# Kernel optimization log

Measured on AMD Instinct MI355X. Metric: run time of the kernel, lower is better.

Reference implementation:

```python
import jax, jax.numpy as jnp
import numpy as np

T, B, H, L = 256, 64, 1024, 2

def setup_inputs() -> dict:
    key = jax.random.key(0)
    ks = jax.random.split(key, 7)
    s = 1.0 / np.sqrt(H)  # torch LSTMCell init scale (uniform); randn*s keeps magnitudes sane
    return {
        "input_seq": jax.random.normal(ks[0], (T, B, H), jnp.float32),
        "h0": jax.random.normal(ks[1], (L, B, H), jnp.float32),
        "c0": jax.random.normal(ks[2], (L, B, H), jnp.float32),
        "W_ih": jax.random.normal(ks[3], (L, 4 * H, H), jnp.float32) * s,
        "W_hh": jax.random.normal(ks[4], (L, 4 * H, H), jnp.float32) * s,
        "b_ih": jax.random.normal(ks[5], (L, 4 * H), jnp.float32) * s,
        "b_hh": jax.random.normal(ks[6], (L, 4 * H), jnp.float32) * s,
    }

def _lstm_cell(x, h, c, w_ih, w_hh, bi, bh):
    # torch.nn.LSTMCell gate order: i, f, g, o
    gates = x @ w_ih.T + bi + h @ w_hh.T + bh  # [B, 4H]
    i, f, g, o = jnp.split(gates, 4, axis=-1)
    c_new = jax.nn.sigmoid(f) * c + jax.nn.sigmoid(i) * jnp.tanh(g)
    h_new = jax.nn.sigmoid(o) * jnp.tanh(c_new)
    return h_new, c_new

def reference(input_seq, h0, c0, W_ih, W_hh, b_ih, b_hh):
    def step(carry, x_t):
        h, c = carry  # each [L, B, H]
        new_h, new_c = [], []
        x = x_t
        for l in range(L):  # small fixed layer loop
            hl, cl = _lstm_cell(x, h[l], c[l], W_ih[l], W_hh[l], b_ih[l], b_hh[l])
            new_h.append(hl)
            new_c.append(cl)
            x = hl
        return (jnp.stack(new_h), jnp.stack(new_c)), None
    (h_fin, c_fin), _ = jax.lax.scan(step, (h0, c0), input_seq)
    return h_fin[-1]  # top-layer hidden at final timestep, [B, H]
```

## Files before the change

kernel.cpp:

```cpp
#include <hip/hip_runtime.h>

#define T_LEN 256
#define B_SZ  64
#define H_SZ  1024
#define G4H   4096
#define HB    (B_SZ * H_SZ)
#define NBLK  256
#define RING_SLOTS (T_LEN + 1)

typedef __attribute__((ext_vector_type(8))) short short8;
typedef __attribute__((ext_vector_type(4))) float float4_;
typedef __attribute__((ext_vector_type(4))) unsigned int uint4_;
typedef __attribute__((ext_vector_type(8))) unsigned int uint8_;

__device__ __forceinline__ unsigned short bf16_rne(float x) {
  unsigned u = __builtin_bit_cast(unsigned, x);
  unsigned r = u + 0x7FFFu + ((u >> 16) & 1u);
  return (unsigned short)(r >> 16);
}
__device__ __forceinline__ float bf16_to_f32(unsigned short s) {
  unsigned u = ((unsigned)s) << 16;
  return __builtin_bit_cast(float, u);
}

__global__ __launch_bounds__(256)
void pack_x(const float* __restrict__ src, unsigned* __restrict__ dst) {
  const size_t i = ((size_t)blockIdx.x * 256 + threadIdx.x) * 4;
  float4_ v = *(const float4_*)(src + i);
  uint4_ o;
  #pragma unroll
  for (int j = 0; j < 4; ++j) {
    const unsigned short h = bf16_rne(v[j]);
    const unsigned short l = bf16_rne(v[j] - bf16_to_f32(h));
    o[j] = (unsigned)h | ((unsigned)l << 16);
  }
  *(uint4_*)(dst + i) = o;
}

__global__ __launch_bounds__(256)
void init_h(const float* __restrict__ h0, unsigned short* __restrict__ ringb,
            unsigned* __restrict__ bar) {
  if (blockIdx.x == 0) {
    #pragma unroll
    for (int j = 0; j < 4; ++j) bar[threadIdx.x * 4 + j] = 0u;
  }
  const int e0 = (blockIdx.x * 256 + threadIdx.x) * 4;
  #pragma unroll
  for (int j = 0; j < 4; ++j) {
    const int e = e0 + j;
    const int l = e >> 16;
    const int rem = e & (HB - 1);
    ringb[((size_t)l * RING_SLOTS + T_LEN) * HB + rem] = bf16_rne(h0[e]);
  }
}

__device__ __forceinline__ void wave_poll64(const unsigned* s64, unsigned v,
                                            int lane) {
  for (;;) {
    const unsigned s = __hip_atomic_load(s64 + lane, __ATOMIC_RELAXED,
                                         __HIP_MEMORY_SCOPE_AGENT);
    if (__all((int)(s >= v))) return;
    __builtin_amdgcn_s_sleep(1);
  }
}

__device__ __forceinline__ void accum_hb(float4_ (&acc)[4][2],
                                         const unsigned short* src,
                                         const short8 (&wp)[2][2][4],
                                         const int nn, const int quad,
                                         const int wave) {
  const int kbase = wave * 128 + quad * 8;
  short8 v[16];
  #pragma unroll
  for (int kb = 0; kb < 4; ++kb)
    #pragma unroll
    for (int m = 0; m < 4; ++m)
      v[kb * 4 + m] = *(const short8*)(src + (size_t)(m * 16 + nn) * H_SZ +
                                       kbase + kb * 32);
  #pragma unroll
  for (int kb = 0; kb < 4; ++kb)
    #pragma unroll
    for (int m = 0; m < 4; ++m)
      #pragma unroll
      for (int nt = 0; nt < 2; ++nt) {
        acc[m][nt] = __builtin_amdgcn_mfma_f32_16x16x32_bf16(v[kb * 4 + m], wp[0][nt][kb], acc[m][nt], 0, 0, 0);
        acc[m][nt] = __builtin_amdgcn_mfma_f32_16x16x32_bf16(v[kb * 4 + m], wp[1][nt][kb], acc[m][nt], 0, 0, 0);
      }
}

__device__ __forceinline__ void accum_xp(float4_ (&acc)[4][2],
                                         const unsigned* src,
                                         const short8 (&wp)[2][2][4],
                                         const int nn, const int quad,
                                         const int wave) {
  #pragma unroll
  for (int kb = 0; kb < 4; ++kb) {
    const int k0 = wave * 128 + kb * 32 + quad * 8;
    #pragma unroll
    for (int m = 0; m < 4; ++m) {
      const uint8_ u = *(const uint8_*)(src + (size_t)(m * 16 + nn) * H_SZ + k0);
      uint4_ h4, l4;
      #pragma unroll
      for (int r = 0; r < 4; ++r) {
        h4[r] = __builtin_amdgcn_perm(u[2 * r + 1], u[2 * r], 0x05040100u);
        l4[r] = __builtin_amdgcn_perm(u[2 * r + 1], u[2 * r], 0x07060302u);
      }
      const short8 hi = __builtin_bit_cast(short8, h4);
      const short8 lo = __builtin_bit_cast(short8, l4);
      #pragma unroll
      for (int nt = 0; nt < 2; ++nt) {
        acc[m][nt] = __builtin_amdgcn_mfma_f32_16x16x32_bf16(hi, wp[0][nt][kb], acc[m][nt], 0, 0, 0);
        acc[m][nt] = __builtin_amdgcn_mfma_f32_16x16x32_bf16(lo, wp[0][nt][kb], acc[m][nt], 0, 0, 0);
        acc[m][nt] = __builtin_amdgcn_mfma_f32_16x16x32_bf16(hi, wp[1][nt][kb], acc[m][nt], 0, 0, 0);
      }
    }
  }
}

__global__ __launch_bounds__(512, 1)
void lstm_persist(const unsigned* __restrict__ xp,
                  const float* __restrict__ c0_in,
                  const float* __restrict__ Wih,
                  const float* __restrict__ Whh,
                  const float* __restrict__ bih,
                  const float* __restrict__ bhh,
                  unsigned short* __restrict__ ringb,
                  float* __restrict__ out,
                  unsigned* __restrict__ bar)
{
  const int wg   = blockIdx.x;
  const int tid  = threadIdx.x;
  const int lane = tid & 63;
  const int wave = tid >> 6;

  const int layer = wg >> 7;
  const int cb    = wg & 127;
  const int nn    = lane & 15;
  const int quad  = lane >> 4;

  __shared__ float lds[2][8][64][36];

  int growA[2];
  #pragma unroll
  for (int nt = 0; nt < 2; ++nt) {
    const int q = nt * 2 + (nn >> 3);
    growA[nt] = q * H_SZ + cb * 8 + (nn & 7);
  }

  short8 wreg[2][2][2][4];
  #pragma unroll
  for (int mat = 0; mat < 2; ++mat) {
    const float* wsrc = mat ? Whh : Wih;
    #pragma unroll
    for (int nt = 0; nt < 2; ++nt)
      #pragma unroll
      for (int kb = 0; kb < 4; ++kb) {
        const float* p = wsrc + ((size_t)layer * G4H + growA[nt]) * H_SZ +
                         wave * 128 + kb * 32 + quad * 8;
        short8 hi, lo;
        #pragma unroll
        for (int j = 0; j < 8; ++j) {
          const float v = p[j];
          const unsigned short h = bf16_rne(v);
          hi[j] = (short)h;
          lo[j] = (short)bf16_rne(v - bf16_to_f32(h));
        }
        wreg[mat][0][nt][kb] = hi;
        wreg[mat][1][nt][kb] = lo;
      }
  }

  const int eb   = wave * 16 + (lane >> 2);
  const int ec   = (lane & 3) * 2;
  const int ecol = cb * 8 + ec;
  float4_ biasA, biasB;
  #pragma unroll
  for (int q = 0; q < 4; ++q) {
    biasA[q] = bih[layer * G4H + q * H_SZ + ecol] +
               bhh[layer * G4H + q * H_SZ + ecol];
    biasB[q] = bih[layer * G4H + q * H_SZ + ecol + 1] +
               bhh[layer * G4H + q * H_SZ + ecol + 1];
  }

  unsigned*       subflag   = bar + layer * 512 + cb * 4 + wave;
  const unsigned* chunk_own = bar + layer * 512 + wave * 64;
  const unsigned* chunk_l0  = bar + wave * 64;

  const unsigned short* ring_own = ringb + (size_t)layer * RING_SLOTS * HB;
  const unsigned short* ring_l0  = ringb;

  float cA = 0.f, cB = 0.f;
  float4_ acc[4][2];
  #pragma unroll
  for (int m = 0; m < 4; ++m)
    #pragma unroll
    for (int nt = 0; nt < 2; ++nt)
      acc[m][nt] = float4_{0.f, 0.f, 0.f, 0.f};

  if (layer == 0) {
    accum_xp(acc, xp, wreg[0], nn, quad, wave);
  } else {
    wave_poll64(chunk_l0, 1u, lane);
    accum_hb(acc, ring_l0 , wreg[0], nn, quad, wave);
  }

  #pragma unroll 1
  for (int t = 0; t < T_LEN; ++t) {
    if (t > 0)
      wave_poll64(chunk_own, (unsigned)t, lane);

    accum_hb(acc, ring_own + (size_t)(t ? t - 1 : T_LEN) * HB,
             wreg[1], nn, quad, wave);

    float (*ldsb)[64][36] = lds[t & 1];
    #pragma unroll
    for (int m = 0; m < 4; ++m)
      #pragma unroll
      for (int nt = 0; nt < 2; ++nt)
        #pragma unroll
        for (int r = 0; r < 4; ++r)
          ldsb[wave][m * 16 + quad * 4 + r]
              [((nn & 7) << 2) + nt * 2 + (nn >> 3)] = acc[m][nt][r];
    __syncthreads();

    if (wave < 4) {
      float4_ gA = biasA, gB = biasB;
      #pragma unroll
      for (int w = 0; w < 8; ++w) {
        gA += *(const float4_*)&ldsb[w][eb][ec * 4];
        gB += *(const float4_*)&ldsb[w][eb][ec * 4 + 4];
      }
      float cpA, cpB;
      if (t == 0) {
        cpA = c0_in[(size_t)layer * HB + (size_t)eb * H_SZ + ecol];
        cpB = c0_in[(size_t)layer * HB + (size_t)eb * H_SZ + ecol + 1];
      } else { cpA = cA; cpB = cB; }
      const float igA = 1.f / (1.f + __expf(-gA[0]));
      const float fgA = 1.f / (1.f + __expf(-gA[1]));
      const float ggA = tanhf(gA[2]);
      const float ogA = 1.f / (1.f + __expf(-gA[3]));
      const float cnA = fgA * cpA + igA * ggA;
      const float hnA = ogA * tanhf(cnA);
      const float igB = 1.f / (1.f + __expf(-gB[0]));
      const float fgB = 1.f / (1.f + __expf(-gB[1]));
      const float ggB = tanhf(gB[2]);
      const float ogB = 1.f / (1.f + __expf(-gB[3]));
      const float cnB = fgB * cpB + igB * ggB;
      const float hnB = ogB * tanhf(cnB);
      cA = cnA; cB = cnB;
      const size_t ridx = ((size_t)layer * RING_SLOTS + t) * HB +
                          (size_t)eb * H_SZ + ecol;
      const unsigned pk = (unsigned)bf16_rne(hnA) |
                          ((unsigned)bf16_rne(hnB) << 16);
      __hip_atomic_store((unsigned*)(ringb + ridx), pk,
                         __ATOMIC_RELAXED, __HIP_MEMORY_SCOPE_AGENT);
      if (layer == 1 && t == T_LEN - 1) {
        out[(size_t)eb * H_SZ + ecol]     = hnA;
        out[(size_t)eb * H_SZ + ecol + 1] = hnB;
      }
      asm volatile("s_waitcnt vmcnt(0)" ::: "memory");
      if (lane == 0)
        __hip_atomic_store(subflag, (unsigned)(t + 1),
                           __ATOMIC_RELAXED, __HIP_MEMORY_SCOPE_AGENT);
    }

    if (t < T_LEN - 1) {
      #pragma unroll
      for (int m = 0; m < 4; ++m)
        #pragma unroll
        for (int nt = 0; nt < 2; ++nt)
          acc[m][nt] = float4_{0.f, 0.f, 0.f, 0.f};
      if (layer == 0) {
        accum_xp(acc, xp + (size_t)(t + 1) * HB, wreg[0], nn, quad, wave);
      } else {
        wave_poll64(chunk_l0, (unsigned)(t + 2), lane);
        accum_hb(acc, ring_l0 + (size_t)(t + 1) * HB,
                 wreg[0], nn, quad, wave);
      }
    }
  }
}

extern "C" void kernel_launch(void* const* d_in, const int* in_sizes, int n_in,
                              void* d_out, int out_size, void* d_ws, size_t ws_size,
                              hipStream_t stream) {
  (void)in_sizes; (void)n_in; (void)out_size; (void)ws_size;
  const float* x   = (const float*)d_in[0];
  const float* h0  = (const float*)d_in[1];
  const float* c0  = (const float*)d_in[2];
  const float* Wih = (const float*)d_in[3];
  const float* Whh = (const float*)d_in[4];
  const float* bih = (const float*)d_in[5];
  const float* bhh = (const float*)d_in[6];
  float* out = (float*)d_out;

  char* w = (char*)d_ws;
  unsigned*       xpack = (unsigned*)w;
  unsigned short* ringb = (unsigned short*)(w + (size_t)T_LEN * HB * 4);
  unsigned*       bar   = (unsigned*)(w + (size_t)T_LEN * HB * 4
                                        + (size_t)2 * RING_SLOTS * HB * 2);

  pack_x<<<(T_LEN * HB) / 4 / 256, 256, 0, stream>>>(x, xpack);
  init_h<<<2 * HB / 4 / 256, 256, 0, stream>>>(h0, ringb, bar);
  lstm_persist<<<NBLK, 512, 0, stream>>>(xpack, c0, Wih, Whh, bih, bhh,
                                         ringb, out, bar);
}
```

Baseline: 3.675 ms.

## Split recurrent GEMM across waves by output tile with full-K and LDS weights

Restructures the recurrent step so each wave owns one 16x16 output tile (batch block by gate-column half) over the full K dimension. W_hh hi/lo parts move to LDS while W_ih stays in registers. This removes the per-step cross-wave LDS reduction and the __syncthreads barrier. The input projection is accumulated into an LDS tile via atomics with a counter. Completion signalling drops from per-wave flags to one flag per block, raised by the last wave through an LDS counter. The change adds LDS weight traffic and shuffle-based gate transposes, and brings spin-wait and race risk on the LDS counters.

```diff
diff --git a/kernel.cpp b/kernel.cpp
--- a/kernel.cpp
+++ b/kernel.cpp
@@ -54,66 +54,15 @@
   }
 }
 
-__device__ __forceinline__ void wave_poll64(const unsigned* s64, unsigned v,
+__device__ __forceinline__ void poll_all128(const unsigned* f, unsigned v,
                                             int lane) {
   for (;;) {
-    const unsigned s = __hip_atomic_load(s64 + lane, __ATOMIC_RELAXED,
+    const unsigned a = __hip_atomic_load(f + lane, __ATOMIC_RELAXED,
                                          __HIP_MEMORY_SCOPE_AGENT);
-    if (__all((int)(s >= v))) return;
+    const unsigned b = __hip_atomic_load(f + 64 + lane, __ATOMIC_RELAXED,
+                                         __HIP_MEMORY_SCOPE_AGENT);
+    if (__all((int)(a >= v && b >= v))) return;
     __builtin_amdgcn_s_sleep(1);
-  }
-}
-
-__device__ __forceinline__ void accum_hb(float4_ (&acc)[4][2],
-                                         const unsigned short* src,
-                                         const short8 (&wp)[2][2][4],
-                                         const int nn, const int quad,
-                                         const int wave) {
-  const int kbase = wave * 128 + quad * 8;
-  short8 v[16];
-  #pragma unroll
-  for (int kb = 0; kb < 4; ++kb)
-    #pragma unroll
-    for (int m = 0; m < 4; ++m)
-      v[kb * 4 + m] = *(const short8*)(src + (size_t)(m * 16 + nn) * H_SZ +
-                                       kbase + kb * 32);
-  #pragma unroll
-  for (int kb = 0; kb < 4; ++kb)
-    #pragma unroll
-    for (int m = 0; m < 4; ++m)
-      #pragma unroll
-      for (int nt = 0; nt < 2; ++nt) {
-        acc[m][nt] = __builtin_amdgcn_mfma_f32_16x16x32_bf16(v[kb * 4 + m], wp[0][nt][kb], acc[m][nt], 0, 0, 0);
-        acc[m][nt] = __builtin_amdgcn_mfma_f32_16x16x32_bf16(v[kb * 4 + m], wp[1][nt][kb], acc[m][nt], 0, 0, 0);
-      }
-}
-
-__device__ __forceinline__ void accum_xp(float4_ (&acc)[4][2],
-                                         const unsigned* src,
-                                         const short8 (&wp)[2][2][4],
-                                         const int nn, const int quad,
-                                         const int wave) {
-  #pragma unroll
-  for (int kb = 0; kb < 4; ++kb) {
-    const int k0 = wave * 128 + kb * 32 + quad * 8;
-    #pragma unroll
-    for (int m = 0; m < 4; ++m) {
-      const uint8_ u = *(const uint8_*)(src + (size_t)(m * 16 + nn) * H_SZ + k0);
-      uint4_ h4, l4;
-      #pragma unroll
-      for (int r = 0; r < 4; ++r) {
-        h4[r] = __builtin_amdgcn_perm(u[2 * r + 1], u[2 * r], 0x05040100u);
-        l4[r] = __builtin_amdgcn_perm(u[2 * r + 1], u[2 * r], 0x07060302u);
-      }
-      const short8 hi = __builtin_bit_cast(short8, h4);
-      const short8 lo = __builtin_bit_cast(short8, l4);
-      #pragma unroll
-      for (int nt = 0; nt < 2; ++nt) {
-        acc[m][nt] = __builtin_amdgcn_mfma_f32_16x16x32_bf16(hi, wp[0][nt][kb], acc[m][nt], 0, 0, 0);
-        acc[m][nt] = __builtin_amdgcn_mfma_f32_16x16x32_bf16(lo, wp[0][nt][kb], acc[m][nt], 0, 0, 0);
-        acc[m][nt] = __builtin_amdgcn_mfma_f32_16x16x32_bf16(hi, wp[1][nt][kb], acc[m][nt], 0, 0, 0);
-      }
-    }
   }
 }
 
@@ -137,26 +86,25 @@
   const int cb    = wg & 127;
   const int nn    = lane & 15;
   const int quad  = lane >> 4;
-
-  __shared__ float lds[2][8][64][36];
-
-  int growA[2];
-  #pragma unroll
-  for (int nt = 0; nt < 2; ++nt) {
-    const int q = nt * 2 + (nn >> 3);
-    growA[nt] = q * H_SZ + cb * 8 + (nn & 7);
-  }
-
-  short8 wreg[2][2][2][4];
-  #pragma unroll
-  for (int mat = 0; mat < 2; ++mat) {
-    const float* wsrc = mat ? Whh : Wih;
-    #pragma unroll
-    for (int nt = 0; nt < 2; ++nt)
-      #pragma unroll
-      for (int kb = 0; kb < 4; ++kb) {
-        const float* p = wsrc + ((size_t)layer * G4H + growA[nt]) * H_SZ +
-                         wave * 128 + kb * 32 + quad * 8;
+  const int m     = wave >> 1;
+  const int nt    = wave & 1;
+  const int g     = lane & 3;
+  const int hcg   = (lane >> 2) & 3;
+
+  __shared__ short8   wh[2][32][2][64];
+  __shared__ float    xtile[2][64][36];
+  __shared__ unsigned cnt, xcnt;
+
+  {
+    const int c = lane & 15;
+    #pragma unroll
+    for (int i = 0; i < 4; ++i) {
+      const int kbg = wave * 4 + i;
+      #pragma unroll
+      for (int ntt = 0; ntt < 2; ++ntt) {
+        const int row = (c & 3) * H_SZ + cb * 8 + ntt * 4 + (c >> 2);
+        const float* p = Whh + ((size_t)layer * G4H + row) * H_SZ +
+                         kbg * 32 + quad * 8;
         short8 hi, lo;
         #pragma unroll
         for (int j = 0; j < 8; ++j) {
@@ -165,119 +113,209 @@
           hi[j] = (short)h;
           lo[j] = (short)bf16_rne(v - bf16_to_f32(h));
         }
-        wreg[mat][0][nt][kb] = hi;
-        wreg[mat][1][nt][kb] = lo;
-      }
-  }
-
-  const int eb   = wave * 16 + (lane >> 2);
-  const int ec   = (lane & 3) * 2;
-  const int ecol = cb * 8 + ec;
-  float4_ biasA, biasB;
+        wh[0][kbg][ntt][lane] = hi;
+        wh[1][kbg][ntt][lane] = lo;
+      }
+    }
+  }
+
+  short8 wx[2][2][4];
+  {
+    const int c = lane & 15;
+    #pragma unroll
+    for (int i = 0; i < 4; ++i)
+      #pragma unroll
+      for (int ntt = 0; ntt < 2; ++ntt) {
+        const int row = (c & 3) * H_SZ + cb * 8 + ntt * 4 + (c >> 2);
+        const float* p = Wih + ((size_t)layer * G4H + row) * H_SZ +
+                         (wave * 4 + i) * 32 + quad * 8;
+        short8 hi, lo;
+        #pragma unroll
+        for (int j = 0; j < 8; ++j) {
+          const float v = p[j];
+          const unsigned short h = bf16_rne(v);
+          hi[j] = (short)h;
+          lo[j] = (short)bf16_rne(v - bf16_to_f32(h));
+        }
+        wx[0][ntt][i] = hi;
+        wx[1][ntt][i] = lo;
+      }
+  }
+
+  const int batch = m * 16 + quad * 4 + g;
+  const int hcol  = cb * 8 + nt * 4 + hcg;
+  float4_ bias4;
   #pragma unroll
-  for (int q = 0; q < 4; ++q) {
-    biasA[q] = bih[layer * G4H + q * H_SZ + ecol] +
-               bhh[layer * G4H + q * H_SZ + ecol];
-    biasB[q] = bih[layer * G4H + q * H_SZ + ecol + 1] +
-               bhh[layer * G4H + q * H_SZ + ecol + 1];
-  }
-
-  unsigned*       subflag   = bar + layer * 512 + cb * 4 + wave;
-  const unsigned* chunk_own = bar + layer * 512 + wave * 64;
-  const unsigned* chunk_l0  = bar + wave * 64;
-
+  for (int q = 0; q < 4; ++q)
+    bias4[q] = bih[layer * G4H + q * H_SZ + hcol] +
+               bhh[layer * G4H + q * H_SZ + hcol];
+
+  unsigned*       slotp = bar + layer * 128 + cb;
+  const unsigned* fown  = bar + layer * 128;
+  const unsigned* fl0   = bar;
   const unsigned short* ring_own = ringb + (size_t)layer * RING_SLOTS * HB;
-  const unsigned short* ring_l0  = ringb;
-
-  float cA = 0.f, cB = 0.f;
-  float4_ acc[4][2];
-  #pragma unroll
-  for (int m = 0; m < 4; ++m)
-    #pragma unroll
-    for (int nt = 0; nt < 2; ++nt)
-      acc[m][nt] = float4_{0.f, 0.f, 0.f, 0.f};
-
-  if (layer == 0) {
-    accum_xp(acc, xp, wreg[0], nn, quad, wave);
-  } else {
-    wave_poll64(chunk_l0, 1u, lane);
-    accum_hb(acc, ring_l0 , wreg[0], nn, quad, wave);
-  }
+
+  {
+    float* z = &xtile[0][0][0];
+    for (int i = tid; i < 2 * 64 * 36; i += 512) z[i] = 0.f;
+    if (tid == 0) { cnt = 0u; xcnt = 0u; }
+  }
+  __syncthreads();
+
+  auto do_shadow = [&](int tt, int buf) {
+    float4_ as[4][2];
+    #pragma unroll
+    for (int mm = 0; mm < 4; ++mm)
+      #pragma unroll
+      for (int ntt = 0; ntt < 2; ++ntt)
+        as[mm][ntt] = float4_{0.f, 0.f, 0.f, 0.f};
+    if (layer == 0) {
+      const unsigned* src = xp + (size_t)tt * HB;
+      #pragma unroll
+      for (int i = 0; i < 4; ++i) {
+        const int k0 = (wave * 4 + i) * 32 + quad * 8;
+        #pragma unroll
+        for (int mm = 0; mm < 4; ++mm) {
+          const uint8_ u = *(const uint8_*)(src + (size_t)(mm * 16 + nn) * H_SZ + k0);
+          uint4_ h4, l4;
+          #pragma unroll
+          for (int r = 0; r < 4; ++r) {
+            h4[r] = __builtin_amdgcn_perm(u[2 * r + 1], u[2 * r], 0x05040100u);
+            l4[r] = __builtin_amdgcn_perm(u[2 * r + 1], u[2 * r], 0x07060302u);
+          }
+          const short8 ah = __builtin_bit_cast(short8, h4);
+          const short8 al = __builtin_bit_cast(short8, l4);
+          #pragma unroll
+          for (int ntt = 0; ntt < 2; ++ntt) {
+            as[mm][ntt] = __builtin_amdgcn_mfma_f32_16x16x32_bf16(ah, wx[0][ntt][i], as[mm][ntt], 0, 0, 0);
+            as[mm][ntt] = __builtin_amdgcn_mfma_f32_16x16x32_bf16(al, wx[0][ntt][i], as[mm][ntt], 0, 0, 0);
+            as[mm][ntt] = __builtin_amdgcn_mfma_f32_16x16x32_bf16(ah, wx[1][ntt][i], as[mm][ntt], 0, 0, 0);
+          }
+        }
+      }
+    } else {
+      poll_all128(fl0, (unsigned)(tt + 1), lane);
+      asm volatile("" ::: "memory");
+      const unsigned short* src = ringb + (size_t)tt * HB;
+      #pragma unroll
+      for (int i = 0; i < 4; ++i) {
+        const int k0 = (wave * 4 + i) * 32 + quad * 8;
+        #pragma unroll
+        for (int mm = 0; mm < 4; ++mm) {
+          const short8 a = *(const short8*)(src + (size_t)(mm * 16 + nn) * H_SZ + k0);
+          #pragma unroll
+          for (int ntt = 0; ntt < 2; ++ntt) {
+            as[mm][ntt] = __builtin_amdgcn_mfma_f32_16x16x32_bf16(a, wx[0][ntt][i], as[mm][ntt], 0, 0, 0);
+            as[mm][ntt] = __builtin_amdgcn_mfma_f32_16x16x32_bf16(a, wx[1][ntt][i], as[mm][ntt], 0, 0, 0);
+          }
+        }
+      }
+    }
+    #pragma unroll
+    for (int mm = 0; mm < 4; ++mm)
+      #pragma unroll
+      for (int ntt = 0; ntt < 2; ++ntt)
+        #pragma unroll
+        for (int r = 0; r < 4; ++r)
+          atomicAdd(&xtile[buf][mm * 16 + quad * 4 + r][ntt * 16 + nn],
+                    as[mm][ntt][r]);
+    asm volatile("s_waitcnt lgkmcnt(0)" ::: "memory");
+    if (lane == 0) atomicAdd(&xcnt, 1u);
+  };
+
+  do_shadow(0, 0);
+
+  float creg = 0.f;
+  volatile unsigned* xcv = &xcnt;
 
   #pragma unroll 1
   for (int t = 0; t < T_LEN; ++t) {
-    if (t > 0)
-      wave_poll64(chunk_own, (unsigned)t, lane);
-
-    accum_hb(acc, ring_own + (size_t)(t ? t - 1 : T_LEN) * HB,
-             wreg[1], nn, quad, wave);
-
-    float (*ldsb)[64][36] = lds[t & 1];
-    #pragma unroll
-    for (int m = 0; m < 4; ++m)
-      #pragma unroll
-      for (int nt = 0; nt < 2; ++nt)
-        #pragma unroll
-        for (int r = 0; r < 4; ++r)
-          ldsb[wave][m * 16 + quad * 4 + r]
-              [((nn & 7) << 2) + nt * 2 + (nn >> 3)] = acc[m][nt][r];
-    __syncthreads();
-
-    if (wave < 4) {
-      float4_ gA = biasA, gB = biasB;
-      #pragma unroll
-      for (int w = 0; w < 8; ++w) {
-        gA += *(const float4_*)&ldsb[w][eb][ec * 4];
-        gB += *(const float4_*)&ldsb[w][eb][ec * 4 + 4];
-      }
-      float cpA, cpB;
-      if (t == 0) {
-        cpA = c0_in[(size_t)layer * HB + (size_t)eb * H_SZ + ecol];
-        cpB = c0_in[(size_t)layer * HB + (size_t)eb * H_SZ + ecol + 1];
-      } else { cpA = cA; cpB = cB; }
-      const float igA = 1.f / (1.f + __expf(-gA[0]));
-      const float fgA = 1.f / (1.f + __expf(-gA[1]));
-      const float ggA = tanhf(gA[2]);
-      const float ogA = 1.f / (1.f + __expf(-gA[3]));
-      const float cnA = fgA * cpA + igA * ggA;
-      const float hnA = ogA * tanhf(cnA);
-      const float igB = 1.f / (1.f + __expf(-gB[0]));
-      const float fgB = 1.f / (1.f + __expf(-gB[1]));
-      const float ggB = tanhf(gB[2]);
-      const float ogB = 1.f / (1.f + __expf(-gB[3]));
-      const float cnB = fgB * cpB + igB * ggB;
-      const float hnB = ogB * tanhf(cnB);
-      cA = cnA; cB = cnB;
-      const size_t ridx = ((size_t)layer * RING_SLOTS + t) * HB +
-                          (size_t)eb * H_SZ + ecol;
-      const unsigned pk = (unsigned)bf16_rne(hnA) |
-                          ((unsigned)bf16_rne(hnB) << 16);
-      __hip_atomic_store((unsigned*)(ringb + ridx), pk,
-                         __ATOMIC_RELAXED, __HIP_MEMORY_SCOPE_AGENT);
-      if (layer == 1 && t == T_LEN - 1) {
-        out[(size_t)eb * H_SZ + ecol]     = hnA;
-        out[(size_t)eb * H_SZ + ecol + 1] = hnB;
-      }
-      asm volatile("s_waitcnt vmcnt(0)" ::: "memory");
-      if (lane == 0)
-        __hip_atomic_store(subflag, (unsigned)(t + 1),
+    if (t > 0) {
+      poll_all128(fown, (unsigned)t, lane);
+      asm volatile("" ::: "memory");
+    }
+
+    const unsigned short* hsrc = ring_own + (size_t)(t ? t - 1 : T_LEN) * HB;
+    float4_ p[4];
+    #pragma unroll
+    for (int i = 0; i < 4; ++i) p[i] = float4_{0.f, 0.f, 0.f, 0.f};
+    #pragma unroll
+    for (int half = 0; half < 2; ++half) {
+      short8 a[16];
+      #pragma unroll
+      for (int i = 0; i < 16; ++i)
+        a[i] = *(const short8*)(hsrc + (size_t)(m * 16 + nn) * H_SZ +
+                                (half * 16 + i) * 32 + quad * 8);
+      #pragma unroll
+      for (int i = 0; i < 16; ++i) {
+        const int kbg = half * 16 + i;
+        const short8 bh = wh[0][kbg][nt][lane];
+        const short8 bl = wh[1][kbg][nt][lane];
+        p[i & 3] = __builtin_amdgcn_mfma_f32_16x16x32_bf16(a[i], bh, p[i & 3], 0, 0, 0);
+        p[i & 3] = __builtin_amdgcn_mfma_f32_16x16x32_bf16(a[i], bl, p[i & 3], 0, 0, 0);
+      }
+    }
+    const float4_ acc = (p[0] + p[1]) + (p[2] + p[3]);
+
+    const float a0 = acc[0], a1 = acc[1], a2 = acc[2], a3 = acc[3];
+    float s0 = (g & 1) ? a0 : a1;
+    float s1 = (g & 1) ? a2 : a3;
+    float r0 = __shfl_xor(s0, 1);
+    float r1 = __shfl_xor(s1, 1);
+    const float b0 = (g & 1) ? r0 : a0;
+    const float b1 = (g & 1) ? a1 : r0;
+    const float b2 = (g & 1) ? r1 : a2;
+    const float b3 = (g & 1) ? a3 : r1;
+    s0 = (g & 2) ? b0 : b2;
+    s1 = (g & 2) ? b1 : b3;
+    r0 = __shfl_xor(s0, 2);
+    r1 = __shfl_xor(s1, 2);
+    const float q0 = (g & 2) ? r0 : b0;
+    const float q1 = (g & 2) ? r1 : b1;
+    const float q2 = (g & 2) ? b2 : r0;
+    const float q3 = (g & 2) ? b3 : r1;
+
+    const unsigned need = 8u * (unsigned)(t + 1);
+    while (*xcv < need) __builtin_amdgcn_s_sleep(1);
+    const int xcol = nt * 16 + hcg * 4;
+    const float4_ xt = *(const float4_*)&xtile[t & 1][batch][xcol];
+    *(float4_*)&xtile[t & 1][batch][xcol] = float4_{0.f, 0.f, 0.f, 0.f};
+
+    const float g0 = q0 + xt[0] + bias4[0];
+    const float g1 = q1 + xt[1] + bias4[1];
+    const float g2 = q2 + xt[2] + bias4[2];
+    const float g3 = q3 + xt[3] + bias4[3];
+    const float cprev = (t == 0)
+        ? c0_in[(size_t)layer * HB + (size_t)batch * H_SZ + hcol] : creg;
+    const float ig = 1.f / (1.f + __expf(-g0));
+    const float fg = 1.f / (1.f + __expf(-g1));
+    const float gg = tanhf(g2);
+    const float og = 1.f / (1.f + __expf(-g3));
+    const float cn = fg * cprev + ig * gg;
+    const float hn = og * tanhf(cn);
+    creg = cn;
+
+    const float hnp = __shfl_xor(hn, 4);
+    if ((lane & 4) == 0) {
+      const unsigned pk = (unsigned)bf16_rne(hn) |
+                          ((unsigned)bf16_rne(hnp) << 16);
+      __hip_atomic_store(
+          (unsigned*)(ringb + ((size_t)layer * RING_SLOTS + t) * HB +
+                      (size_t)batch * H_SZ + hcol),
+          pk, __ATOMIC_RELAXED, __HIP_MEMORY_SCOPE_AGENT);
+    }
+    if (layer == 1 && t == T_LEN - 1)
+      out[(size_t)batch * H_SZ + hcol] = hn;
+
+    asm volatile("s_waitcnt vmcnt(0) lgkmcnt(0)" ::: "memory");
+    if (lane == 0) {
+      const unsigned old = atomicAdd(&cnt, 1u);
+      if (old == 8u * (unsigned)t + 7u)
+        __hip_atomic_store(slotp, (unsigned)(t + 1),
                            __ATOMIC_RELAXED, __HIP_MEMORY_SCOPE_AGENT);
     }
 
-    if (t < T_LEN - 1) {
-      #pragma unroll
-      for (int m = 0; m < 4; ++m)
-        #pragma unroll
-        for (int nt = 0; nt < 2; ++nt)
-          acc[m][nt] = float4_{0.f, 0.f, 0.f, 0.f};
-      if (layer == 0) {
-        accum_xp(acc, xp + (size_t)(t + 1) * HB, wreg[0], nn, quad, wave);
-      } else {
-        wave_poll64(chunk_l0, (unsigned)(t + 2), lane);
-        accum_hb(acc, ring_l0 + (size_t)(t + 1) * HB,
-                 wreg[0], nn, quad, wave);
-      }
-    }
+    if (t < T_LEN - 1) do_shadow(t + 1, (t + 1) & 1);
   }
 }
 
```

Result: slower. 8.448 ms (+129.9%).

## Split barrier polling into finer groups and rebalance input-side K across waves

Applied to the files above, without the earlier changes.

Each wave now polls only the producer flags for the batch row group it is about to load, and issues those loads right after that group's flags are ready instead of waiting on one 64-flag check. The input-side (W_ih) GEMM is redistributed unevenly: waves 0-3 take 3 K-blocks and waves 4-7 take 5. This offloads waves 0-3, which also run the gate epilogue. Layer 1 waits only on the layer-0 flags covering its own K range. The aim is to shorten the critical path between timesteps and balance per-wave work, at the cost of more complex polling and a variable register footprint for the input weights.

```diff
diff --git a/kernel.cpp b/kernel.cpp
--- a/kernel.cpp
+++ b/kernel.cpp
@@ -54,66 +54,27 @@
   }
 }
 
-__device__ __forceinline__ void wave_poll64(const unsigned* s64, unsigned v,
-                                            int lane) {
+__device__ __forceinline__ void poll_mgrp(const unsigned* chunk, int m,
+                                          unsigned v, int lane) {
+  const unsigned* p = chunk + ((lane & 15) << 2) + m;
   for (;;) {
-    const unsigned s = __hip_atomic_load(s64 + lane, __ATOMIC_RELAXED,
+    const unsigned s = __hip_atomic_load(p, __ATOMIC_RELAXED,
                                          __HIP_MEMORY_SCOPE_AGENT);
     if (__all((int)(s >= v))) return;
     __builtin_amdgcn_s_sleep(1);
   }
 }
 
-__device__ __forceinline__ void accum_hb(float4_ (&acc)[4][2],
-                                         const unsigned short* src,
-                                         const short8 (&wp)[2][2][4],
-                                         const int nn, const int quad,
-                                         const int wave) {
-  const int kbase = wave * 128 + quad * 8;
-  short8 v[16];
-  #pragma unroll
-  for (int kb = 0; kb < 4; ++kb)
-    #pragma unroll
-    for (int m = 0; m < 4; ++m)
-      v[kb * 4 + m] = *(const short8*)(src + (size_t)(m * 16 + nn) * H_SZ +
-                                       kbase + kb * 32);
-  #pragma unroll
-  for (int kb = 0; kb < 4; ++kb)
-    #pragma unroll
-    for (int m = 0; m < 4; ++m)
-      #pragma unroll
-      for (int nt = 0; nt < 2; ++nt) {
-        acc[m][nt] = __builtin_amdgcn_mfma_f32_16x16x32_bf16(v[kb * 4 + m], wp[0][nt][kb], acc[m][nt], 0, 0, 0);
-        acc[m][nt] = __builtin_amdgcn_mfma_f32_16x16x32_bf16(v[kb * 4 + m], wp[1][nt][kb], acc[m][nt], 0, 0, 0);
-      }
-}
-
-__device__ __forceinline__ void accum_xp(float4_ (&acc)[4][2],
-                                         const unsigned* src,
-                                         const short8 (&wp)[2][2][4],
-                                         const int nn, const int quad,
-                                         const int wave) {
-  #pragma unroll
-  for (int kb = 0; kb < 4; ++kb) {
-    const int k0 = wave * 128 + kb * 32 + quad * 8;
-    #pragma unroll
-    for (int m = 0; m < 4; ++m) {
-      const uint8_ u = *(const uint8_*)(src + (size_t)(m * 16 + nn) * H_SZ + k0);
-      uint4_ h4, l4;
-      #pragma unroll
-      for (int r = 0; r < 4; ++r) {
-        h4[r] = __builtin_amdgcn_perm(u[2 * r + 1], u[2 * r], 0x05040100u);
-        l4[r] = __builtin_amdgcn_perm(u[2 * r + 1], u[2 * r], 0x07060302u);
-      }
-      const short8 hi = __builtin_bit_cast(short8, h4);
-      const short8 lo = __builtin_bit_cast(short8, l4);
-      #pragma unroll
-      for (int nt = 0; nt < 2; ++nt) {
-        acc[m][nt] = __builtin_amdgcn_mfma_f32_16x16x32_bf16(hi, wp[0][nt][kb], acc[m][nt], 0, 0, 0);
-        acc[m][nt] = __builtin_amdgcn_mfma_f32_16x16x32_bf16(lo, wp[0][nt][kb], acc[m][nt], 0, 0, 0);
-        acc[m][nt] = __builtin_amdgcn_mfma_f32_16x16x32_bf16(hi, wp[1][nt][kb], acc[m][nt], 0, 0, 0);
-      }
-    }
+__device__ __forceinline__ void poll_range(const unsigned* f, int n,
+                                           unsigned v, int lane) {
+  for (;;) {
+    unsigned a = 0xFFFFFFFFu, b = 0xFFFFFFFFu;
+    if (lane < n) a = __hip_atomic_load(f + lane, __ATOMIC_RELAXED,
+                                        __HIP_MEMORY_SCOPE_AGENT);
+    if (lane + 64 < n) b = __hip_atomic_load(f + lane + 64, __ATOMIC_RELAXED,
+                                             __HIP_MEMORY_SCOPE_AGENT);
+    if (__all((int)(a >= v && b >= v))) return;
+    __builtin_amdgcn_s_sleep(1);
   }
 }
 
@@ -147,27 +108,45 @@
     growA[nt] = q * H_SZ + cb * 8 + (nn & 7);
   }
 
-  short8 wreg[2][2][2][4];
-  #pragma unroll
-  for (int mat = 0; mat < 2; ++mat) {
-    const float* wsrc = mat ? Whh : Wih;
-    #pragma unroll
-    for (int nt = 0; nt < 2; ++nt)
-      #pragma unroll
-      for (int kb = 0; kb < 4; ++kb) {
-        const float* p = wsrc + ((size_t)layer * G4H + growA[nt]) * H_SZ +
-                         wave * 128 + kb * 32 + quad * 8;
-        short8 hi, lo;
-        #pragma unroll
-        for (int j = 0; j < 8; ++j) {
-          const float v = p[j];
-          const unsigned short h = bf16_rne(v);
-          hi[j] = (short)h;
-          lo[j] = (short)bf16_rne(v - bf16_to_f32(h));
-        }
-        wreg[mat][0][nt][kb] = hi;
-        wreg[mat][1][nt][kb] = lo;
-      }
+  short8 wh[2][2][4];
+  #pragma unroll
+  for (int nt = 0; nt < 2; ++nt)
+    #pragma unroll
+    for (int kb = 0; kb < 4; ++kb) {
+      const float* p = Whh + ((size_t)layer * G4H + growA[nt]) * H_SZ +
+                       wave * 128 + kb * 32 + quad * 8;
+      short8 hi, lo;
+      #pragma unroll
+      for (int j = 0; j < 8; ++j) {
+        const float v = p[j];
+        const unsigned short h = bf16_rne(v);
+        hi[j] = (short)h;
+        lo[j] = (short)bf16_rne(v - bf16_to_f32(h));
+      }
+      wh[0][nt][kb] = hi;
+      wh[1][nt][kb] = lo;
+    }
+
+  const int kbstart = (wave < 4) ? wave * 3 : 12 + (wave - 4) * 5;
+  const int nkb     = (wave < 4) ? 3 : 5;
+  short8 wx[2][2][5];
+  #pragma unroll
+  for (int i = 0; i < 5; ++i) if (i < nkb) {
+    #pragma unroll
+    for (int nt = 0; nt < 2; ++nt) {
+      const float* p = Wih + ((size_t)layer * G4H + growA[nt]) * H_SZ +
+                       (kbstart + i) * 32 + quad * 8;
+      short8 hi, lo;
+      #pragma unroll
+      for (int j = 0; j < 8; ++j) {
+        const float v = p[j];
+        const unsigned short h = bf16_rne(v);
+        hi[j] = (short)h;
+        lo[j] = (short)bf16_rne(v - bf16_to_f32(h));
+      }
+      wx[0][nt][i] = hi;
+      wx[1][nt][i] = lo;
+    }
   }
 
   const int eb   = wave * 16 + (lane >> 2);
@@ -184,7 +163,7 @@
 
   unsigned*       subflag   = bar + layer * 512 + cb * 4 + wave;
   const unsigned* chunk_own = bar + layer * 512 + wave * 64;
-  const unsigned* chunk_l0  = bar + wave * 64;
+  const unsigned* fl0sub    = bar;
 
   const unsigned short* ring_own = ringb + (size_t)layer * RING_SLOTS * HB;
   const unsigned short* ring_l0  = ringb;
@@ -197,20 +176,79 @@
     for (int nt = 0; nt < 2; ++nt)
       acc[m][nt] = float4_{0.f, 0.f, 0.f, 0.f};
 
-  if (layer == 0) {
-    accum_xp(acc, xp, wreg[0], nn, quad, wave);
-  } else {
-    wave_poll64(chunk_l0, 1u, lane);
-    accum_hb(acc, ring_l0 , wreg[0], nn, quad, wave);
-  }
+  auto xside = [&](int tt) {
+    if (layer == 0) {
+      const unsigned* src = xp + (size_t)tt * HB;
+      #pragma unroll
+      for (int i = 0; i < 5; ++i) if (i < nkb) {
+        const int k0 = (kbstart + i) * 32 + quad * 8;
+        #pragma unroll
+        for (int m = 0; m < 4; ++m) {
+          const uint8_ u = *(const uint8_*)(src + (size_t)(m * 16 + nn) * H_SZ + k0);
+          uint4_ h4, l4;
+          #pragma unroll
+          for (int r = 0; r < 4; ++r) {
+            h4[r] = __builtin_amdgcn_perm(u[2 * r + 1], u[2 * r], 0x05040100u);
+            l4[r] = __builtin_amdgcn_perm(u[2 * r + 1], u[2 * r], 0x07060302u);
+          }
+          const short8 ah = __builtin_bit_cast(short8, h4);
+          const short8 al = __builtin_bit_cast(short8, l4);
+          #pragma unroll
+          for (int nt = 0; nt < 2; ++nt) {
+            acc[m][nt] = __builtin_amdgcn_mfma_f32_16x16x32_bf16(ah, wx[0][nt][i], acc[m][nt], 0, 0, 0);
+            acc[m][nt] = __builtin_amdgcn_mfma_f32_16x16x32_bf16(al, wx[0][nt][i], acc[m][nt], 0, 0, 0);
+            acc[m][nt] = __builtin_amdgcn_mfma_f32_16x16x32_bf16(ah, wx[1][nt][i], acc[m][nt], 0, 0, 0);
+          }
+        }
+      }
+    } else {
+      poll_range(fl0sub + kbstart * 16, nkb * 16, (unsigned)(tt + 1), lane);
+      asm volatile("" ::: "memory");
+      const unsigned short* src = ring_l0 + (size_t)tt * HB;
+      #pragma unroll
+      for (int i = 0; i < 5; ++i) if (i < nkb) {
+        const int k0 = (kbstart + i) * 32 + quad * 8;
+        #pragma unroll
+        for (int m = 0; m < 4; ++m) {
+          const short8 a = *(const short8*)(src + (size_t)(m * 16 + nn) * H_SZ + k0);
+          #pragma unroll
+          for (int nt = 0; nt < 2; ++nt) {
+            acc[m][nt] = __builtin_amdgcn_mfma_f32_16x16x32_bf16(a, wx[0][nt][i], acc[m][nt], 0, 0, 0);
+            acc[m][nt] = __builtin_amdgcn_mfma_f32_16x16x32_bf16(a, wx[1][nt][i], acc[m][nt], 0, 0, 0);
+          }
+        }
+      }
+    }
+  };
+
+  xside(0);
 
   #pragma unroll 1
   for (int t = 0; t < T_LEN; ++t) {
-    if (t > 0)
-      wave_poll64(chunk_own, (unsigned)t, lane);
-
-    accum_hb(acc, ring_own + (size_t)(t ? t - 1 : T_LEN) * HB,
-             wreg[1], nn, quad, wave);
+    {
+      const unsigned short* hsrc =
+          ring_own + (size_t)(t ? t - 1 : T_LEN) * HB;
+      const int kbase = wave * 128 + quad * 8;
+      short8 v[16];
+      #pragma unroll
+      for (int m = 0; m < 4; ++m) {
+        if (t > 0) poll_mgrp(chunk_own, m, (unsigned)t, lane);
+        #pragma unroll
+        for (int kb = 0; kb < 4; ++kb)
+          v[m * 4 + kb] = *(const short8*)(hsrc +
+                              (size_t)(m * 16 + nn) * H_SZ + kbase + kb * 32);
+      }
+      asm volatile("" ::: "memory");
+      #pragma unroll
+      for (int kb = 0; kb < 4; ++kb)
+        #pragma unroll
+        for (int m = 0; m < 4; ++m)
+          #pragma unroll
+          for (int nt = 0; nt < 2; ++nt) {
+            acc[m][nt] = __builtin_amdgcn_mfma_f32_16x16x32_bf16(v[m * 4 + kb], wh[0][nt][kb], acc[m][nt], 0, 0, 0);
+            acc[m][nt] = __builtin_amdgcn_mfma_f32_16x16x32_bf16(v[m * 4 + kb], wh[1][nt][kb], acc[m][nt], 0, 0, 0);
+          }
+    }
 
     float (*ldsb)[64][36] = lds[t & 1];
     #pragma unroll
@@ -270,13 +308,7 @@
         #pragma unroll
         for (int nt = 0; nt < 2; ++nt)
           acc[m][nt] = float4_{0.f, 0.f, 0.f, 0.f};
-      if (layer == 0) {
-        accum_xp(acc, xp + (size_t)(t + 1) * HB, wreg[0], nn, quad, wave);
-      } else {
-        wave_poll64(chunk_l0, (unsigned)(t + 2), lane);
-        accum_hb(acc, ring_l0 + (size_t)(t + 1) * HB,
-                 wreg[0], nn, quad, wave);
-      }
+      xside(t + 1);
     }
   }
 }
```

Measured after the change: 3.802 ms. +3.5%, slower.
